# Kernel tuning notes

Hardware: AMD Instinct MI355X
Metric: run time of the kernel (lower is better)

Reference implementation:

```python
import jax, jax.numpy as jnp
import numpy as np

EPS = 1e-06
FP8_MAX = 448.0  # float8_e4m3fn max
T, H = 8192, 4096


def setup_inputs() -> dict:
    key = jax.random.key(0)
    ks = jax.random.split(key, 5)
    return {
        "hidden_states": jax.random.normal(ks[0], (T, H), dtype=jnp.float32),
        "norm_w": jax.random.uniform(ks[1], (4, H), dtype=jnp.float32),
        "w": jax.random.uniform(ks[2], (3, H, H), dtype=jnp.float32),
        "wscale": jax.random.uniform(ks[3], (3,), dtype=jnp.float32),
        "scale": jax.random.uniform(ks[4], (3,), dtype=jnp.float32),
    }


def _rmsnorm(x, g):
    var = jnp.mean(x * x, axis=-1, keepdims=True)
    return x * jax.lax.rsqrt(var + EPS) * g


def _fp8_quant(x, s):
    # static per-tensor quant: scale, clamp to fp8 range, cast to e4m3 and back
    q = jnp.clip(x / s, -FP8_MAX, FP8_MAX)
    return q.astype(jnp.float8_e4m3fn).astype(jnp.float32)


def _fp8_linear(x, wq, s_in, s_w):
    qx = _fp8_quant(x, s_in)
    return (qx @ wq) * (s_in * s_w)


def reference(hidden_states, norm_w, w, wscale, scale):
    # weight fp8 quantization (module stores weights already in fp8)
    wq = w.astype(jnp.float8_e4m3fn).astype(jnp.float32)  # [3,H,H]

    z = jax.nn.relu(hidden_states)
    x = resid = z  # all_reduce == identity on one device
    y = _rmsnorm(x, norm_w[0])

    z2 = _fp8_linear(y, wq[0], scale[0], wscale[0])
    x2 = z2 + resid
    resid = x2
    y2 = _rmsnorm(x2, norm_w[1])

    z3 = _fp8_linear(y2, wq[1], scale[1], wscale[1])
    x3 = z3 + resid
    resid = x3
    y3 = _rmsnorm(x3, norm_w[2])

    z4 = _fp8_linear(y3, wq[2], scale[2], wscale[2])
    x4 = z4 + resid
    y4 = _rmsnorm(x4, norm_w[3])
    return y4
```

## Files before the change

### kernel.cpp

```cpp
#include <hip/hip_runtime.h>

typedef float f32x4  __attribute__((ext_vector_type(4)));
typedef float f32x16 __attribute__((ext_vector_type(16)));
typedef int   i32x4  __attribute__((ext_vector_type(4)));
typedef int   i32x8  __attribute__((ext_vector_type(8)));

#define T_DIM 8192
#define H_DIM 4096
#define SC1 0x7f7f7f7f

__device__ __forceinline__ unsigned int pack_fp8x4(float a, float b, float c, float d) {
    int v = __builtin_amdgcn_cvt_pk_fp8_f32(a, b, 0, false);
    v = __builtin_amdgcn_cvt_pk_fp8_f32(c, d, v, true);
    return (unsigned int)v;
}


__global__ __launch_bounds__(256) void wquant_kernel(
    const float* __restrict__ w, unsigned char* __restrict__ wqT)
{
    const int l  = blockIdx.z;
    const int n0 = blockIdx.x * 64;
    const int k0 = blockIdx.y * 64;
    const int tid = threadIdx.x;
    __shared__ unsigned char tile[64][68];
    const float* wl = w + (size_t)l * H_DIM * H_DIM;
#pragma unroll
    for (int p = 0; p < 4; ++p) {
        int r = p * 16 + (tid >> 4);
        int c = (tid & 15) * 4;
        f32x4 v = *(const f32x4*)(wl + (size_t)(k0 + r) * H_DIM + n0 + c);
        *(unsigned int*)&tile[r][c] = pack_fp8x4(v[0], v[1], v[2], v[3]);
    }
    __syncthreads();
    const int nl = tid >> 2;
    const int g  = tid & 3;
    unsigned int words[4];
#pragma unroll
    for (int wi = 0; wi < 4; ++wi) {
        unsigned int a = 0;
#pragma unroll
        for (int b = 0; b < 4; ++b)
            a |= (unsigned int)tile[g * 16 + wi * 4 + b][nl] << (8 * b);
        words[wi] = a;
    }
    unsigned char* op = wqT + ((size_t)l * H_DIM + n0 + nl) * H_DIM + k0 + g * 16;
    uint4 ov; ov.x = words[0]; ov.y = words[1]; ov.z = words[2]; ov.w = words[3];
    *(uint4*)op = ov;
}

template <int MODE>
__global__ __launch_bounds__(256) void row_kernel(
    const float* __restrict__ in,
    float* __restrict__ resid_out,
    void* __restrict__ out,
    const float* __restrict__ g,
    const float* __restrict__ scale_p)
{
    const int row = blockIdx.x;
    const int tid = threadIdx.x;
    const float* rin = in + (size_t)row * H_DIM;
    float x[16];
    float ss = 0.0f;
#pragma unroll
    for (int j = 0; j < 4; ++j) {
        const int base = (j * 256 + tid) * 4;
        f32x4 v = *(const f32x4*)(rin + base);
        f32x4 rv;
#pragma unroll
        for (int i = 0; i < 4; ++i) {
            float t = v[i];
            if (MODE == 0) t = fmaxf(t, 0.0f);
            x[j * 4 + i] = t;
            rv[i] = t;
            ss += t * t;
        }
        if (MODE == 0)
            *(f32x4*)(resid_out + (size_t)row * H_DIM + base) = rv;
    }
#pragma unroll
    for (int off = 32; off > 0; off >>= 1)
        ss += __shfl_down(ss, off, 64);
    __shared__ float red[4];
    if ((tid & 63) == 0) red[tid >> 6] = ss;
    __syncthreads();
    const float var  = (red[0] + red[1] + red[2] + red[3]) * (1.0f / (float)H_DIM);
    const float rinv = 1.0f / sqrtf(var + 1e-6f);

    if (MODE == 2) {
        float* ro = (float*)out + (size_t)row * H_DIM;
#pragma unroll
        for (int j = 0; j < 4; ++j) {
            const int base = (j * 256 + tid) * 4;
            f32x4 gv = *(const f32x4*)(g + base);
            f32x4 ov;
#pragma unroll
            for (int i = 0; i < 4; ++i) ov[i] = (x[j * 4 + i] * rinv) * gv[i];
            *(f32x4*)(ro + base) = ov;
        }
    } else {
        const float s = scale_p[0];
        unsigned int* qo = (unsigned int*)out + (size_t)row * (H_DIM / 4);
#pragma unroll
        for (int j = 0; j < 4; ++j) {
            const int base = (j * 256 + tid) * 4;
            f32x4 gv = *(const f32x4*)(g + base);
            float q[4];
#pragma unroll
            for (int i = 0; i < 4; ++i) {
                float y = (x[j * 4 + i] * rinv) * gv[i];
                y = y / s;
                q[i] = fminf(fmaxf(y, -448.0f), 448.0f);
            }
            qo[j * 256 + tid] = pack_fp8x4(q[0], q[1], q[2], q[3]);
        }
    }
}

__device__ __forceinline__ void stage_half(const unsigned char* gsrc, unsigned char* ldsdst) {
    __builtin_amdgcn_global_load_lds(
        (const __attribute__((address_space(1))) unsigned int*)gsrc,
        (__attribute__((address_space(3))) unsigned int*)ldsdst, 16, 0, 0);
}

#define VM4 asm volatile("s_waitcnt vmcnt(4)" ::: "memory")
#define VM0 asm volatile("s_waitcnt vmcnt(0)" ::: "memory")

#define MM2(m) do {                                                             \
    acc[m][0] = __builtin_amdgcn_mfma_scale_f32_32x32x64_f8f6f4(                \
        fa[m], fb[0], acc[m][0], 0, 0, 0, SC1, 0, SC1);                         \
    acc[m][1] = __builtin_amdgcn_mfma_scale_f32_32x32x64_f8f6f4(                \
        fa[m], fb[1], acc[m][1], 0, 0, 0, SC1, 0, SC1);                         \
} while (0)

#define RDA(OR, m) do {                                                         \
    *(i32x4*)&fa[m]        = *(const i32x4*)(lds + (OR) + wrA + (m) * 2048 + fo0); \
    *(((i32x4*)&fa[m]) + 1) = *(const i32x4*)(lds + (OR) + wrA + (m) * 2048 + fo1); \
} while (0)

#define RDB(OR) do {                                                            \
    _Pragma("unroll") for (int n = 0; n < 2; ++n) {                             \
        *(i32x4*)&fb[n]        = *(const i32x4*)(lds + (OR) + wcB + n * 2048 + fo0); \
        *(((i32x4*)&fb[n]) + 1) = *(const i32x4*)(lds + (OR) + wcB + n * 2048 + fo1); \
    }                                                                           \
} while (0)

#define ITER(STG, VMW, OR, OS) do {                                             \
    if (STG) {                                                                  \
        stage_half(bA  + (kt2 + voff), lds + (OS) + 0     + wave * 1024);       \
        stage_half(bAh + (kt2 + voff), lds + (OS) + 8192  + wave * 1024);       \
        stage_half(bB  + (kt2 + voff), lds + (OS) + 16384 + wave * 1024);       \
        stage_half(bBh + (kt2 + voff), lds + (OS) + 24576 + wave * 1024);       \
        kt2 += 64;                                                              \
    }                                                                           \
    VMW;                                                                        \
    __builtin_amdgcn_s_barrier();                                               \
    MM2(0); MM2(1);                                                             \
    RDA(OR, 0); RDA(OR, 1);                                                     \
    MM2(2); MM2(3);                                                             \
    RDA(OR, 2); RDA(OR, 3); RDB(OR);                                            \
    __builtin_amdgcn_sched_group_barrier(0x008, 4, 0);                          \
    __builtin_amdgcn_sched_group_barrier(0x100, 4, 0);                          \
    __builtin_amdgcn_sched_group_barrier(0x008, 4, 0);                          \
    __builtin_amdgcn_sched_group_barrier(0x100, 8, 0);                          \
} while (0)

__global__ __launch_bounds__(512, 2) void gemm_fp8_kernel(
    const unsigned char* __restrict__ A,
    const unsigned char* __restrict__ B,
    float* __restrict__ C,
    const float* __restrict__ s_in,
    const float* __restrict__ s_w)
{
    __shared__ unsigned char lds[98304];

    const float alpha = s_in[0] * s_w[0];

    const int b = blockIdx.x;
    const int local = b >> 3, chunk = b & 7;
    const int bm = (chunk & 3) * 8 + (local & 7);
    const int bn = (chunk >> 2) * 8 + (local >> 3);

    const int tid  = threadIdx.x;
    const int wave = tid >> 6;
    const int lane = tid & 63;
    const int wr   = wave >> 2;
    const int wc   = wave & 3;

    const int sw  = (lane >> 1) & 3;
    const int fo0 = (lane & 31) * 64 + ((((lane >> 5) * 2) + 0 ^ sw)) * 16;
    const int fo1 = (lane & 31) * 64 + ((((lane >> 5) * 2) + 1 ^ sw)) * 16;
    const int wrA = wr * 8192;
    const int wcB = 16384 + wc * 4096;

    const int voff = (tid >> 2) * H_DIM + ((tid & 3) ^ ((tid >> 3) & 3)) * 16;
    const unsigned char* bA  = A + (size_t)bm * 256 * H_DIM;
    const unsigned char* bAh = bA + (size_t)128 * H_DIM;
    const unsigned char* bB  = B + (size_t)bn * 256 * H_DIM;
    const unsigned char* bBh = bB + (size_t)128 * H_DIM;

    f32x16 acc[4][2];
#pragma unroll
    for (int m = 0; m < 4; ++m)
#pragma unroll
        for (int n = 0; n < 2; ++n)
#pragma unroll
            for (int e = 0; e < 16; ++e) acc[m][n][e] = 0.0f;

    i32x8 fa[4], fb[2];
    int kt2;

    stage_half(bA  + voff, lds + 0     + wave * 1024);
    stage_half(bAh + voff, lds + 8192  + wave * 1024);
    stage_half(bB  + voff, lds + 16384 + wave * 1024);
    stage_half(bBh + voff, lds + 24576 + wave * 1024);
    stage_half(bA  + (voff + 64), lds + 32768 + 0     + wave * 1024);
    stage_half(bAh + (voff + 64), lds + 32768 + 8192  + wave * 1024);
    stage_half(bB  + (voff + 64), lds + 32768 + 16384 + wave * 1024);
    stage_half(bBh + (voff + 64), lds + 32768 + 24576 + wave * 1024);
    VM4;
    __builtin_amdgcn_s_barrier();
    RDA(0, 0); RDA(0, 1); RDA(0, 2); RDA(0, 3); RDB(0);
    kt2 = 128;

#pragma unroll 1
    for (int t3 = 0; t3 < 60; t3 += 3) {
        ITER(1, VM4, 32768, 65536);
        ITER(1, VM4, 65536, 0);
        ITER(1, VM4, 0,     32768);
    }
    ITER(1, VM4, 32768, 65536);
    ITER(1, VM4, 65536, 0);
    ITER(0, VM0, 0,     0);
    MM2(0); MM2(1); MM2(2); MM2(3);

    const int lrow0 = bm * 256 + wr * 128 + 4 * (lane >> 5);
    const int lcol0 = bn * 256 + wc * 64 + (lane & 31);
#pragma unroll
    for (int m = 0; m < 4; ++m) {
#pragma unroll
        for (int n = 0; n < 2; ++n) {
#pragma unroll
            for (int e = 0; e < 16; ++e) {
                const int row = lrow0 + m * 32 + (e & 3) + 8 * (e >> 2);
                float* cp = C + (size_t)row * H_DIM + lcol0 + n * 32;
                *cp = acc[m][n][e] * alpha + *cp;
            }
        }
    }
}

extern "C" void kernel_launch(void* const* d_in, const int* in_sizes, int n_in,
                              void* d_out, int out_size, void* d_ws, size_t ws_size,
                              hipStream_t stream) {
    const float* h   = (const float*)d_in[0];
    const float* nw  = (const float*)d_in[1];
    const float* w   = (const float*)d_in[2];
    const float* wsc = (const float*)d_in[3];
    const float* sc  = (const float*)d_in[4];
    float* out = (float*)d_out;

    unsigned char* wqT = (unsigned char*)d_ws;
    unsigned char* qx  = wqT + (size_t)3 * H_DIM * H_DIM;
    float* resid = (float*)(qx + (size_t)T_DIM * H_DIM);

    const size_t WSTRIDE = (size_t)H_DIM * H_DIM;

    wquant_kernel<<<dim3(64, 64, 3), 256, 0, stream>>>(w, wqT);

    row_kernel<0><<<T_DIM, 256, 0, stream>>>(h, resid, qx, nw + 0 * H_DIM, sc + 0);
    gemm_fp8_kernel<<<512, 512, 0, stream>>>(qx, wqT + 0 * WSTRIDE, resid, sc + 0, wsc + 0);

    row_kernel<1><<<T_DIM, 256, 0, stream>>>(resid, nullptr, qx, nw + 1 * H_DIM, sc + 1);
    gemm_fp8_kernel<<<512, 512, 0, stream>>>(qx, wqT + 1 * WSTRIDE, resid, sc + 1, wsc + 1);

    row_kernel<1><<<T_DIM, 256, 0, stream>>>(resid, nullptr, qx, nw + 2 * H_DIM, sc + 2);
    gemm_fp8_kernel<<<512, 512, 0, stream>>>(qx, wqT + 2 * WSTRIDE, resid, sc + 2, wsc + 2);

    row_kernel<2><<<T_DIM, 256, 0, stream>>>(resid, nullptr, out, nw + 3 * H_DIM, nullptr);
}
```

Before: 647.0 us.

## Pre-swizzle fp8 weights into MFMA fragment order and load B directly to registers

The weight-quant kernel now writes the transposed fp8 weights in a blocked layout that matches each wave's MFMA B-fragment, so the GEMM loads B operands straight from global memory into registers instead of staging them through LDS. Only A is staged via LDS, now with a six-slot ring buffer and deeper prefetch (two k-steps per iteration, vmcnt(8)), and MFMA issue is wrapped in s_setprio. This is meant to cut LDS traffic and barriers per k-step. In exchange it uses more registers for double-buffered B fragments, and direct global B loads may expose latency.

```diff
diff --git a/kernel.cpp b/kernel.cpp
--- a/kernel.cpp
+++ b/kernel.cpp
@@ -44,7 +44,12 @@
             a |= (unsigned int)tile[g * 16 + wi * 4 + b][nl] << (8 * b);
         words[wi] = a;
     }
-    unsigned char* op = wqT + ((size_t)l * H_DIM + n0 + nl) * H_DIM + k0 + g * 16;
+    const int bn = n0 >> 8, wc = (n0 >> 6) & 3, kt = k0 >> 6;
+    const int n2 = nl >> 5;
+    const int lane = (g >> 1) * 32 + (nl & 31);
+    const int byte0 = (g & 1) * 16;
+    const size_t off = ((((size_t)l * 16 + bn) * 64 + kt) * 4 + wc) * 2 + n2;
+    unsigned char* op = wqT + off * 2048 + lane * 32 + byte0;
     uint4 ov; ov.x = words[0]; ov.y = words[1]; ov.z = words[2]; ov.w = words[3];
     *(uint4*)op = ov;
 }
@@ -123,46 +128,59 @@
         (__attribute__((address_space(3))) unsigned int*)ldsdst, 16, 0, 0);
 }
 
+#define VM8 asm volatile("s_waitcnt vmcnt(8)" ::: "memory")
 #define VM4 asm volatile("s_waitcnt vmcnt(4)" ::: "memory")
 #define VM0 asm volatile("s_waitcnt vmcnt(0)" ::: "memory")
-
-#define MM2(m) do {                                                             \
+#define BAR __builtin_amdgcn_s_barrier()
+#define PRIO1 __builtin_amdgcn_s_setprio(1)
+#define PRIO0 __builtin_amdgcn_s_setprio(0)
+
+#define MM2(m, S) do {                                                          \
     acc[m][0] = __builtin_amdgcn_mfma_scale_f32_32x32x64_f8f6f4(                \
-        fa[m], fb[0], acc[m][0], 0, 0, 0, SC1, 0, SC1);                         \
+        fa[m], b##S##0, acc[m][0], 0, 0, 0, SC1, 0, SC1);                       \
     acc[m][1] = __builtin_amdgcn_mfma_scale_f32_32x32x64_f8f6f4(                \
-        fa[m], fb[1], acc[m][1], 0, 0, 0, SC1, 0, SC1);                         \
-} while (0)
-
-#define RDA(OR, m) do {                                                         \
-    *(i32x4*)&fa[m]        = *(const i32x4*)(lds + (OR) + wrA + (m) * 2048 + fo0); \
-    *(((i32x4*)&fa[m]) + 1) = *(const i32x4*)(lds + (OR) + wrA + (m) * 2048 + fo1); \
-} while (0)
-
-#define RDB(OR) do {                                                            \
-    _Pragma("unroll") for (int n = 0; n < 2; ++n) {                             \
-        *(i32x4*)&fb[n]        = *(const i32x4*)(lds + (OR) + wcB + n * 2048 + fo0); \
-        *(((i32x4*)&fb[n]) + 1) = *(const i32x4*)(lds + (OR) + wcB + n * 2048 + fo1); \
-    }                                                                           \
-} while (0)
-
-#define ITER(STG, VMW, OR, OS) do {                                             \
-    if (STG) {                                                                  \
-        stage_half(bA  + (kt2 + voff), lds + (OS) + 0     + wave * 1024);       \
-        stage_half(bAh + (kt2 + voff), lds + (OS) + 8192  + wave * 1024);       \
-        stage_half(bB  + (kt2 + voff), lds + (OS) + 16384 + wave * 1024);       \
-        stage_half(bBh + (kt2 + voff), lds + (OS) + 24576 + wave * 1024);       \
-        kt2 += 64;                                                              \
-    }                                                                           \
-    VMW;                                                                        \
-    __builtin_amdgcn_s_barrier();                                               \
-    MM2(0); MM2(1);                                                             \
-    RDA(OR, 0); RDA(OR, 1);                                                     \
-    MM2(2); MM2(3);                                                             \
-    RDA(OR, 2); RDA(OR, 3); RDB(OR);                                            \
+        fa[m], b##S##1, acc[m][1], 0, 0, 0, SC1, 0, SC1);                       \
+} while (0)
+
+#define RDA(BUF, m) do {                                                        \
+    *(i32x4*)&fa[m]         = *(const i32x4*)(lds + (BUF) + wrA + (m) * 2048 + fo0); \
+    *(((i32x4*)&fa[m]) + 1) = *(const i32x4*)(lds + (BUF) + wrA + (m) * 2048 + fo1); \
+} while (0)
+
+#define TILEBODY(S, BR) do {                                                    \
+    PRIO1; MM2(0, S); PRIO0; RDA(BR, 0);                                        \
+    PRIO1; MM2(1, S); PRIO0; RDA(BR, 1);                                        \
+    PRIO1; MM2(2, S); PRIO0; RDA(BR, 2);                                        \
+    PRIO1; MM2(3, S); PRIO0; RDA(BR, 3);                                        \
     __builtin_amdgcn_sched_group_barrier(0x008, 4, 0);                          \
     __builtin_amdgcn_sched_group_barrier(0x100, 4, 0);                          \
     __builtin_amdgcn_sched_group_barrier(0x008, 4, 0);                          \
-    __builtin_amdgcn_sched_group_barrier(0x100, 8, 0);                          \
+    __builtin_amdgcn_sched_group_barrier(0x100, 4, 0);                          \
+} while (0)
+
+#define TILELAST(S) do {                                                        \
+    PRIO1; MM2(0, S); MM2(1, S); MM2(2, S); MM2(3, S); PRIO0;                   \
+} while (0)
+
+#define LDB(NX) do {                                                            \
+    bE##NX##0 = *(const i32x8*)(gB0 + kb);                                      \
+    bE##NX##1 = *(const i32x8*)(gB0 + kb + 2048);                               \
+    bO##NX##0 = *(const i32x8*)(gB0 + kb + 16384);                              \
+    bO##NX##1 = *(const i32x8*)(gB0 + kb + 16384 + 2048);                       \
+    kb += 32768;                                                                \
+} while (0)
+
+#define STG(KOFF, BUF) do {                                                     \
+    stage_half(gAlo + (KOFF), lds + (BUF) + wave * 1024);                       \
+    stage_half(gAhi + (KOFF), lds + (BUF) + 8192 + wave * 1024);                \
+} while (0)
+
+#define ITER(CU, NX, BR1, BR2, BS1, BS2) do {                                   \
+    LDB(NX);                                                                    \
+    STG(ka, BS1); STG(ka + 64, BS2); ka += 128;                                 \
+    VM8; BAR;                                                                   \
+    TILEBODY(E##CU, BR1);                                                       \
+    TILEBODY(O##CU, BR2);                                                       \
 } while (0)
 
 __global__ __launch_bounds__(512, 2) void gemm_fp8_kernel(
@@ -191,13 +209,13 @@
     const int fo0 = (lane & 31) * 64 + ((((lane >> 5) * 2) + 0 ^ sw)) * 16;
     const int fo1 = (lane & 31) * 64 + ((((lane >> 5) * 2) + 1 ^ sw)) * 16;
     const int wrA = wr * 8192;
-    const int wcB = 16384 + wc * 4096;
 
     const int voff = (tid >> 2) * H_DIM + ((tid & 3) ^ ((tid >> 3) & 3)) * 16;
-    const unsigned char* bA  = A + (size_t)bm * 256 * H_DIM;
-    const unsigned char* bAh = bA + (size_t)128 * H_DIM;
-    const unsigned char* bB  = B + (size_t)bn * 256 * H_DIM;
-    const unsigned char* bBh = bB + (size_t)128 * H_DIM;
+    const unsigned char* gAlo = A + (size_t)bm * 256 * H_DIM + voff;
+    const unsigned char* gAhi = gAlo + (size_t)128 * H_DIM;
+
+    const unsigned char* gB0 =
+        B + ((((size_t)bn * 64) * 4 + wc) * 2) * 2048 + lane * 32;
 
     f32x16 acc[4][2];
 #pragma unroll
@@ -207,32 +225,35 @@
 #pragma unroll
             for (int e = 0; e < 16; ++e) acc[m][n][e] = 0.0f;
 
-    i32x8 fa[4], fb[2];
-    int kt2;
-
-    stage_half(bA  + voff, lds + 0     + wave * 1024);
-    stage_half(bAh + voff, lds + 8192  + wave * 1024);
-    stage_half(bB  + voff, lds + 16384 + wave * 1024);
-    stage_half(bBh + voff, lds + 24576 + wave * 1024);
-    stage_half(bA  + (voff + 64), lds + 32768 + 0     + wave * 1024);
-    stage_half(bAh + (voff + 64), lds + 32768 + 8192  + wave * 1024);
-    stage_half(bB  + (voff + 64), lds + 32768 + 16384 + wave * 1024);
-    stage_half(bBh + (voff + 64), lds + 32768 + 24576 + wave * 1024);
-    VM4;
-    __builtin_amdgcn_s_barrier();
-    RDA(0, 0); RDA(0, 1); RDA(0, 2); RDA(0, 3); RDB(0);
-    kt2 = 128;
+    i32x8 fa[4];
+    i32x8 bEA0, bEA1, bOA0, bOA1, bEB0, bEB1, bOB0, bOB1;
+    int ka, kb;
+
+    STG(0,   0);
+    STG(64,  16384);
+    STG(128, 32768);
+    STG(192, 49152);
+    kb = 0; LDB(A);
+    VM0; BAR;
+    RDA(0, 0); RDA(0, 1); RDA(0, 2); RDA(0, 3);
+    ka = 256;
 
 #pragma unroll 1
-    for (int t3 = 0; t3 < 60; t3 += 3) {
-        ITER(1, VM4, 32768, 65536);
-        ITER(1, VM4, 65536, 0);
-        ITER(1, VM4, 0,     32768);
-    }
-    ITER(1, VM4, 32768, 65536);
-    ITER(1, VM4, 65536, 0);
-    ITER(0, VM0, 0,     0);
-    MM2(0); MM2(1); MM2(2); MM2(3);
+    for (int it = 0; it < 5; ++it) {
+        ITER(A, B, 16384, 32768, 65536, 81920);
+        ITER(B, A, 49152, 65536, 0,     16384);
+        ITER(A, B, 81920, 0,     32768, 49152);
+        ITER(B, A, 16384, 32768, 65536, 81920);
+        ITER(A, B, 49152, 65536, 0,     16384);
+        ITER(B, A, 81920, 0,     32768, 49152);
+    }
+    LDB(B);
+    VM4; BAR;
+    TILEBODY(EA, 16384);
+    TILEBODY(OA, 32768);
+    VM0; BAR;
+    TILEBODY(EB, 49152);
+    TILELAST(OB);
 
     const int lrow0 = bm * 256 + wr * 128 + 4 * (lane >> 5);
     const int lcol0 = bn * 256 + wc * 64 + (lane & 31);
```

New measurement: 754.9 us. 1.17x slower.
